# Performance work log

Measured on AMD Instinct MI355X. Metric: run time of the kernel, lower is better.

The kernel has to match this reference:

```python
import jax, jax.numpy as jnp
import numpy as np

DIM = 128
HEADS = 4


def setup_inputs() -> dict:
    key = jax.random.key(0)
    ks = jax.random.split(key, 6)
    B_, N, C = 2048, 49, DIM
    nW = 64
    x = jax.random.normal(ks[0], (B_, N, C), dtype=jnp.float32)
    mask = jax.random.normal(ks[1], (nW, N, N), dtype=jnp.float32)
    qkv_w = jax.random.normal(ks[2], (3 * C, C), dtype=jnp.float32) * 0.02
    qkv_b = jnp.zeros((3 * C,), dtype=jnp.float32)
    proj_w = jax.random.normal(ks[3], (C, C), dtype=jnp.float32) * 0.02
    proj_b = jnp.zeros((C,), dtype=jnp.float32)
    return {"x": x, "mask": mask, "qkv_w": qkv_w, "qkv_b": qkv_b,
            "proj_w": proj_w, "proj_b": proj_b}


def reference(x, mask, qkv_w, qkv_b, proj_w, proj_b):
    B_, N, C = x.shape
    H = HEADS
    Dh = C // H
    scale = Dh ** (-0.5)
    # fused QKV projection: [B_, N, 3C]
    qkv = x @ qkv_w.T + qkv_b
    qkv = qkv.reshape(B_, N, 3, H, Dh).transpose(2, 0, 3, 1, 4)  # [3, B_, H, N, Dh]
    q, k, v = qkv[0] * scale, qkv[1], qkv[2]
    attn = jnp.einsum('bhqd,bhkd->bhqk', q, k)  # [B_, H, N, N]
    nW = mask.shape[0]
    # add per-window additive mask: broadcast over images and heads
    attn = attn.reshape(B_ // nW, nW, H, N, N) + mask[None, :, None, :, :]
    attn = jax.nn.softmax(attn.reshape(B_, H, N, N), axis=-1)
    out = jnp.einsum('bhqk,bhkd->bhqd', attn, v)  # [B_, H, N, Dh]
    out = out.transpose(0, 2, 1, 3).reshape(B_, N, C)
    return out @ proj_w.T + proj_b
```

## Files before the change

kernel.cpp:

```cpp
#include <hip/hip_runtime.h>

typedef __bf16 bf16_t;
typedef __bf16 bf16x2 __attribute__((ext_vector_type(2)));
typedef __bf16 bf16x4 __attribute__((ext_vector_type(4)));
typedef __bf16 bf16x8 __attribute__((ext_vector_type(8)));
typedef float  f32x4  __attribute__((ext_vector_type(4)));

#define MFMA16(a, b, c) __builtin_amdgcn_mfma_f32_16x16x32_bf16((a), (b), (c), 0, 0, 0)

#define SMEM_BYTES 76800


__global__ void wconv_kernel(const float* __restrict__ qw, const float* __restrict__ pw,
                             bf16_t* __restrict__ o) {
    int i = (blockIdx.x * 256 + threadIdx.x) * 4;
    const float* src = (i < 49152) ? (qw + i) : (pw + (i - 49152));
    float4 f = *(const float4*)src;
    bf16x4 h;
    h[0] = (bf16_t)f.x; h[1] = (bf16_t)f.y; h[2] = (bf16_t)f.z; h[3] = (bf16_t)f.w;
    *(bf16x4*)(o + i) = h;
}

__device__ __forceinline__ bf16x8 ldw(const float* __restrict__ wf,
                                      const bf16_t* __restrict__ wb,
                                      int use_b, int idx) {
    if (use_b) {
        return *(const bf16x8*)(wb + idx);
    } else {
        float4 f0 = *(const float4*)(wf + idx);
        float4 f1 = *(const float4*)(wf + idx + 4);
        bf16x8 r;
        r[0] = (bf16_t)f0.x; r[1] = (bf16_t)f0.y; r[2] = (bf16_t)f0.z; r[3] = (bf16_t)f0.w;
        r[4] = (bf16_t)f1.x; r[5] = (bf16_t)f1.y; r[6] = (bf16_t)f1.z; r[7] = (bf16_t)f1.w;
        return r;
    }
}

__global__ __launch_bounds__(512, 4) void winattn_kernel(
    const float* __restrict__ xg, const float* __restrict__ maskg,
    const float* __restrict__ qwg, const float* __restrict__ qbg,
    const float* __restrict__ pwg, const float* __restrict__ pbg,
    const bf16_t* __restrict__ wqb, const bf16_t* __restrict__ wpb,
    const int use_wbf, const int nW, float* __restrict__ outg)
{
    extern __shared__ char smem[];
    bf16_t* xatt  = (bf16_t*)smem;
    float*  maskl = (float*)smem;

    const int b    = blockIdx.x;
    const int tid  = threadIdx.x;
    const int w    = tid >> 6;
    const int lane = tid & 63;
    const int g    = lane >> 4;
    const int c0   = lane & 15;

    {
        const float4* xb = (const float4*)(xg + (long)b * 6272);
        #pragma unroll 4
        for (int i = tid; i < 1568; i += 512) {
            float4 f = xb[i];
            int row = i >> 5;
            int col = (i & 31) << 2;
            bf16x4 h;
            h[0] = (bf16_t)f.x; h[1] = (bf16_t)f.y; h[2] = (bf16_t)f.z; h[3] = (bf16_t)f.w;
            *(bf16x4*)(xatt + row * 136 + col) = h;
        }
        unsigned int* z = (unsigned int*)(xatt + 49 * 136);
        for (int i = tid; i < 1020; i += 512) z[i] = 0u;
    }
    __syncthreads();

    {
        f32x4 acc[3][4];
        #pragma unroll
        for (int nt = 0; nt < 3; ++nt)
            #pragma unroll
            for (int mt = 0; mt < 4; ++mt) acc[nt][mt] = {0.f, 0.f, 0.f, 0.f};

        #pragma unroll
        for (int ks = 0; ks < 4; ++ks) {
            bf16x8 a[4];
            #pragma unroll
            for (int mt = 0; mt < 4; ++mt)
                a[mt] = *(const bf16x8*)(xatt + (mt * 16 + c0) * 136 + ks * 32 + g * 8);
            #pragma unroll
            for (int nt = 0; nt < 3; ++nt) {
                int o   = (w * 3 + nt) * 16 + c0;
                bf16x8 bb = ldw(qwg, wqb, use_wbf, o * 128 + ks * 32 + g * 8);
                #pragma unroll
                for (int mt = 0; mt < 4; ++mt)
                    acc[nt][mt] = MFMA16(a[mt], bb, acc[nt][mt]);
            }
        }
        #pragma unroll
        for (int nt = 0; nt < 3; ++nt) {
            int og   = (w * 3 + nt) * 16;
            float bias = qbg[og + c0];
            int part = og >> 7;
            int rem  = og & 127;
            int hh   = rem >> 5;
            int dh   = (rem & 31) + c0;
            bf16_t* hb = (bf16_t*)(smem + 17408 + hh * 14848);
            #pragma unroll
            for (int mt = 0; mt < 4; ++mt) {
                #pragma unroll
                for (int r = 0; r < 4; ++r) {
                    int row   = mt * 16 + g * 4 + r;
                    float val = acc[nt][mt][r] + bias;
                    if (part == 0)      hb[row * 40 + dh]        = (bf16_t)val;
                    else if (part == 1) hb[2560 + row * 40 + dh] = (bf16_t)val;
                    else                hb[5120 + dh * 72 + row] = (bf16_t)val;
                }
            }
        }
    }
    __syncthreads();

    {
        const float* mb = maskg + (long)(b % nW) * 2401;
        for (int i = tid; i < 2401; i += 512)
            maskl[(i / 49) * 52 + (i % 49)] = mb[i];
    }
    __syncthreads();

    const int h   = w >> 1;
    const int qh2 = w & 1;
    bf16_t* qls = (bf16_t*)(smem + 17408 + h * 14848);
    bf16_t* kls = qls + 2560;
    bf16_t* vls = qls + 5120;
    bf16_t* pls = qls;
    bf16x8 ka[4], qb2[2];
    #pragma unroll
    for (int mt = 0; mt < 4; ++mt)
        ka[mt] = *(const bf16x8*)(kls + (mt * 16 + c0) * 40 + g * 8);
    #pragma unroll
    for (int nt = 0; nt < 2; ++nt)
        qb2[nt] = *(const bf16x8*)(qls + ((qh2 * 2 + nt) * 16 + c0) * 40 + g * 8);
    __syncthreads();

    {
        f32x4 s[2][4];
        #pragma unroll
        for (int nt = 0; nt < 2; ++nt)
            #pragma unroll
            for (int mt = 0; mt < 4; ++mt) s[nt][mt] = {0.f, 0.f, 0.f, 0.f};
        #pragma unroll
        for (int nt = 0; nt < 2; ++nt)
            #pragma unroll
            for (int mt = 0; mt < 4; ++mt)
                s[nt][mt] = MFMA16(ka[mt], qb2[nt], s[nt][mt]);

        const float scale = 0.17677669529663687f;
        #pragma unroll
        for (int nt = 0; nt < 2; ++nt) {
            int q  = (qh2 * 2 + nt) * 16 + c0;
            int qm = q < 49 ? q : 48;
            float lg[16];
            float m = -1e30f;
            #pragma unroll
            for (int mt = 0; mt < 4; ++mt) {
                #pragma unroll
                for (int r = 0; r < 4; ++r) {
                    int kv  = mt * 16 + g * 4 + r;
                    float v = (kv < 49) ? (s[nt][mt][r] * scale + maskl[qm * 52 + kv])
                                        : -1e30f;
                    lg[mt * 4 + r] = v;
                    m = fmaxf(m, v);
                }
            }
            m = fmaxf(m, __shfl_xor(m, 16));
            m = fmaxf(m, __shfl_xor(m, 32));
            float sum = 0.f;
            #pragma unroll
            for (int i = 0; i < 16; ++i) { float e = __expf(lg[i] - m); lg[i] = e; sum += e; }
            sum += __shfl_xor(sum, 16);
            sum += __shfl_xor(sum, 32);
            float inv = 1.f / sum;
            #pragma unroll
            for (int mt = 0; mt < 4; ++mt) {
                #pragma unroll
                for (int j = 0; j < 2; ++j) {
                    bf16x2 t;
                    t[0] = (bf16_t)(lg[mt * 4 + 2 * j    ] * inv);
                    t[1] = (bf16_t)(lg[mt * 4 + 2 * j + 1] * inv);
                    *(bf16x2*)(pls + q * 72 + mt * 16 + g * 4 + 2 * j) = t;
                }
            }
        }
    }
    __syncthreads();

    {
        f32x4 oo[2][2];
        #pragma unroll
        for (int mt = 0; mt < 2; ++mt)
            #pragma unroll
            for (int nt = 0; nt < 2; ++nt) oo[mt][nt] = {0.f, 0.f, 0.f, 0.f};
        #pragma unroll
        for (int ks = 0; ks < 2; ++ks) {
            bf16x8 va[2], pb2[2];
            #pragma unroll
            for (int mt = 0; mt < 2; ++mt)
                va[mt] = *(const bf16x8*)(vls + (mt * 16 + c0) * 72 + ks * 32 + g * 8);
            #pragma unroll
            for (int nt = 0; nt < 2; ++nt)
                pb2[nt] = *(const bf16x8*)(pls + ((qh2 * 2 + nt) * 16 + c0) * 72 + ks * 32 + g * 8);
            #pragma unroll
            for (int mt = 0; mt < 2; ++mt)
                #pragma unroll
                for (int nt = 0; nt < 2; ++nt)
                    oo[mt][nt] = MFMA16(va[mt], pb2[nt], oo[mt][nt]);
        }
        #pragma unroll
        for (int nt = 0; nt < 2; ++nt) {
            int q = (qh2 * 2 + nt) * 16 + c0;
            #pragma unroll
            for (int mt = 0; mt < 2; ++mt) {
                #pragma unroll
                for (int j = 0; j < 2; ++j) {
                    bf16x2 t;
                    t[0] = (bf16_t)oo[mt][nt][2 * j];
                    t[1] = (bf16_t)oo[mt][nt][2 * j + 1];
                    *(bf16x2*)(xatt + q * 136 + h * 32 + mt * 16 + g * 4 + 2 * j) = t;
                }
            }
        }
    }
    __syncthreads();

    {
        f32x4 acc[4];
        #pragma unroll
        for (int mt = 0; mt < 4; ++mt) acc[mt] = {0.f, 0.f, 0.f, 0.f};
        int col = w * 16 + c0;
        #pragma unroll
        for (int ks = 0; ks < 4; ++ks) {
            bf16x8 a[4];
            #pragma unroll
            for (int mt = 0; mt < 4; ++mt)
                a[mt] = *(const bf16x8*)(xatt + (mt * 16 + c0) * 136 + ks * 32 + g * 8);
            bf16x8 bb = ldw(pwg, wpb, use_wbf, col * 128 + ks * 32 + g * 8);
            #pragma unroll
            for (int mt = 0; mt < 4; ++mt)
                acc[mt] = MFMA16(a[mt], bb, acc[mt]);
        }
        float pb = pbg[col];
        float* ob = outg + (long)b * 6272;
        #pragma unroll
        for (int mt = 0; mt < 4; ++mt) {
            #pragma unroll
            for (int r = 0; r < 4; ++r) {
                int q = mt * 16 + g * 4 + r;
                if (q < 49) ob[q * 128 + col] = acc[mt][r] + pb;
            }
        }
    }
}

extern "C" void kernel_launch(void* const* d_in, const int* in_sizes, int n_in,
                              void* d_out, int out_size, void* d_ws, size_t ws_size,
                              hipStream_t stream) {
    const float* xg  = (const float*)d_in[0];
    const float* mg  = (const float*)d_in[1];
    const float* qwg = (const float*)d_in[2];
    const float* qbg = (const float*)d_in[3];
    const float* pwg = (const float*)d_in[4];
    const float* pbg = (const float*)d_in[5];
    float* outg = (float*)d_out;

    const int B  = in_sizes[0] / (49 * 128);
    const int nW = in_sizes[1] / (49 * 49);

    int use_wbf = (d_ws != nullptr && ws_size >= 131072) ? 1 : 0;
    bf16_t* wqb = (bf16_t*)d_ws;
    bf16_t* wpb = use_wbf ? (wqb + 49152) : nullptr;
    if (use_wbf)
        wconv_kernel<<<64, 256, 0, stream>>>(qwg, pwg, wqb);

    (void)hipFuncSetAttribute((const void*)winattn_kernel,
                              hipFuncAttributeMaxDynamicSharedMemorySize, SMEM_BYTES);

    winattn_kernel<<<B, 512, SMEM_BYTES, stream>>>(
        xg, mg, qwg, qbg, pwg, pbg, wqb, use_wbf ? wpb : wqb, use_wbf, nW, outg);
}
```

Before: 75.12 us.

## Drop weight-convert kernel, swap MFMA operands, load mask into registers, vectorize stores

After: 87.71 us. 1.17x slower.

```diff
diff --git a/kernel.cpp b/kernel.cpp
--- a/kernel.cpp
+++ b/kernel.cpp
@@ -1,7 +1,6 @@
 #include <hip/hip_runtime.h>
 
 typedef __bf16 bf16_t;
-typedef __bf16 bf16x2 __attribute__((ext_vector_type(2)));
 typedef __bf16 bf16x4 __attribute__((ext_vector_type(4)));
 typedef __bf16 bf16x8 __attribute__((ext_vector_type(8)));
 typedef float  f32x4  __attribute__((ext_vector_type(4)));
@@ -11,41 +10,23 @@
 #define SMEM_BYTES 76800
 
 
-__global__ void wconv_kernel(const float* __restrict__ qw, const float* __restrict__ pw,
-                             bf16_t* __restrict__ o) {
-    int i = (blockIdx.x * 256 + threadIdx.x) * 4;
-    const float* src = (i < 49152) ? (qw + i) : (pw + (i - 49152));
-    float4 f = *(const float4*)src;
-    bf16x4 h;
-    h[0] = (bf16_t)f.x; h[1] = (bf16_t)f.y; h[2] = (bf16_t)f.z; h[3] = (bf16_t)f.w;
-    *(bf16x4*)(o + i) = h;
-}
-
-__device__ __forceinline__ bf16x8 ldw(const float* __restrict__ wf,
-                                      const bf16_t* __restrict__ wb,
-                                      int use_b, int idx) {
-    if (use_b) {
-        return *(const bf16x8*)(wb + idx);
-    } else {
-        float4 f0 = *(const float4*)(wf + idx);
-        float4 f1 = *(const float4*)(wf + idx + 4);
-        bf16x8 r;
-        r[0] = (bf16_t)f0.x; r[1] = (bf16_t)f0.y; r[2] = (bf16_t)f0.z; r[3] = (bf16_t)f0.w;
-        r[4] = (bf16_t)f1.x; r[5] = (bf16_t)f1.y; r[6] = (bf16_t)f1.z; r[7] = (bf16_t)f1.w;
-        return r;
-    }
+__device__ __forceinline__ bf16x8 ld8f(const float* __restrict__ p) {
+    float4 f0 = *(const float4*)p;
+    float4 f1 = *(const float4*)(p + 4);
+    bf16x8 r;
+    r[0] = (bf16_t)f0.x; r[1] = (bf16_t)f0.y; r[2] = (bf16_t)f0.z; r[3] = (bf16_t)f0.w;
+    r[4] = (bf16_t)f1.x; r[5] = (bf16_t)f1.y; r[6] = (bf16_t)f1.z; r[7] = (bf16_t)f1.w;
+    return r;
 }
 
 __global__ __launch_bounds__(512, 4) void winattn_kernel(
     const float* __restrict__ xg, const float* __restrict__ maskg,
     const float* __restrict__ qwg, const float* __restrict__ qbg,
     const float* __restrict__ pwg, const float* __restrict__ pbg,
-    const bf16_t* __restrict__ wqb, const bf16_t* __restrict__ wpb,
-    const int use_wbf, const int nW, float* __restrict__ outg)
+    const int nW, float* __restrict__ outg)
 {
     extern __shared__ char smem[];
-    bf16_t* xatt  = (bf16_t*)smem;
-    float*  maskl = (float*)smem;
+    bf16_t* xatt = (bf16_t*)smem;
 
     const int b    = blockIdx.x;
     const int tid  = threadIdx.x;
@@ -71,6 +52,12 @@
     __syncthreads();
 
     {
+        const int orow0 = 48 * w;
+        float4 bias[3];
+        #pragma unroll
+        for (int nt = 0; nt < 3; ++nt)
+            bias[nt] = *(const float4*)(qbg + orow0 + 16 * nt + 4 * g);
+
         f32x4 acc[3][4];
         #pragma unroll
         for (int nt = 0; nt < 3; ++nt)
@@ -79,47 +66,50 @@
 
         #pragma unroll
         for (int ks = 0; ks < 4; ++ks) {
-            bf16x8 a[4];
-            #pragma unroll
-            for (int mt = 0; mt < 4; ++mt)
-                a[mt] = *(const bf16x8*)(xatt + (mt * 16 + c0) * 136 + ks * 32 + g * 8);
-            #pragma unroll
-            for (int nt = 0; nt < 3; ++nt) {
-                int o   = (w * 3 + nt) * 16 + c0;
-                bf16x8 bb = ldw(qwg, wqb, use_wbf, o * 128 + ks * 32 + g * 8);
+            bf16x8 wfk[3];
+            #pragma unroll
+            for (int nt = 0; nt < 3; ++nt)
+                wfk[nt] = ld8f(qwg + (orow0 + 16 * nt + c0) * 128 + 32 * ks + 8 * g);
+            bf16x8 xf[4];
+            #pragma unroll
+            for (int mt = 0; mt < 4; ++mt)
+                xf[mt] = *(const bf16x8*)(xatt + (16 * mt + c0) * 136 + 32 * ks + 8 * g);
+            #pragma unroll
+            for (int nt = 0; nt < 3; ++nt)
                 #pragma unroll
                 for (int mt = 0; mt < 4; ++mt)
-                    acc[nt][mt] = MFMA16(a[mt], bb, acc[nt][mt]);
-            }
-        }
+                    acc[nt][mt] = MFMA16(wfk[nt], xf[mt], acc[nt][mt]);
+        }
+
         #pragma unroll
         for (int nt = 0; nt < 3; ++nt) {
-            int og   = (w * 3 + nt) * 16;
-            float bias = qbg[og + c0];
-            int part = og >> 7;
-            int rem  = og & 127;
+            int o0   = orow0 + 16 * nt + 4 * g;
+            int part = (orow0 + 16 * nt) >> 7;
+            int rem  = o0 & 127;
             int hh   = rem >> 5;
-            int dh   = (rem & 31) + c0;
+            int dh0  = rem & 31;
             bf16_t* hb = (bf16_t*)(smem + 17408 + hh * 14848);
             #pragma unroll
             for (int mt = 0; mt < 4; ++mt) {
-                #pragma unroll
-                for (int r = 0; r < 4; ++r) {
-                    int row   = mt * 16 + g * 4 + r;
-                    float val = acc[nt][mt][r] + bias;
-                    if (part == 0)      hb[row * 40 + dh]        = (bf16_t)val;
-                    else if (part == 1) hb[2560 + row * 40 + dh] = (bf16_t)val;
-                    else                hb[5120 + dh * 72 + row] = (bf16_t)val;
+                int tok = 16 * mt + c0;
+                bf16x4 t;
+                t[0] = (bf16_t)(acc[nt][mt][0] + bias[nt].x);
+                t[1] = (bf16_t)(acc[nt][mt][1] + bias[nt].y);
+                t[2] = (bf16_t)(acc[nt][mt][2] + bias[nt].z);
+                t[3] = (bf16_t)(acc[nt][mt][3] + bias[nt].w);
+                if (part == 0) {
+                    *(bf16x4*)(hb + tok * 40 + dh0) = t;
+                } else if (part == 1) {
+                    *(bf16x4*)(hb + 2560 + tok * 40 + dh0) = t;
+                } else {
+                    bf16_t* vt = hb + 5120;
+                    vt[(dh0 + 0) * 72 + tok] = t[0];
+                    vt[(dh0 + 1) * 72 + tok] = t[1];
+                    vt[(dh0 + 2) * 72 + tok] = t[2];
+                    vt[(dh0 + 3) * 72 + tok] = t[3];
                 }
             }
         }
-    }
-    __syncthreads();
-
-    {
-        const float* mb = maskg + (long)(b % nW) * 2401;
-        for (int i = tid; i < 2401; i += 512)
-            maskl[(i / 49) * 52 + (i % 49)] = mb[i];
     }
     __syncthreads();
 
@@ -129,45 +119,56 @@
     bf16_t* kls = qls + 2560;
     bf16_t* vls = qls + 5120;
     bf16_t* pls = qls;
+
+    float mvals[2][16];
+    {
+        const float* mrow = maskg + (long)(b % nW) * 2401;
+        #pragma unroll
+        for (int nt = 0; nt < 2; ++nt) {
+            int q  = (qh2 * 2 + nt) * 16 + c0;
+            int qm = q < 49 ? q : 48;
+            const float* mr = mrow + qm * 49;
+            #pragma unroll
+            for (int mt = 0; mt < 4; ++mt)
+                #pragma unroll
+                for (int r = 0; r < 4; ++r) {
+                    int kv = 16 * mt + 4 * g + r;
+                    mvals[nt][mt * 4 + r] = (kv < 49) ? mr[kv] : -1e30f;
+                }
+        }
+    }
+
     bf16x8 ka[4], qb2[2];
     #pragma unroll
     for (int mt = 0; mt < 4; ++mt)
-        ka[mt] = *(const bf16x8*)(kls + (mt * 16 + c0) * 40 + g * 8);
+        ka[mt] = *(const bf16x8*)(kls + (16 * mt + c0) * 40 + 8 * g);
     #pragma unroll
     for (int nt = 0; nt < 2; ++nt)
-        qb2[nt] = *(const bf16x8*)(qls + ((qh2 * 2 + nt) * 16 + c0) * 40 + g * 8);
-    __syncthreads();
-
-    {
-        f32x4 s[2][4];
-        #pragma unroll
-        for (int nt = 0; nt < 2; ++nt)
-            #pragma unroll
-            for (int mt = 0; mt < 4; ++mt) s[nt][mt] = {0.f, 0.f, 0.f, 0.f};
-        #pragma unroll
-        for (int nt = 0; nt < 2; ++nt)
-            #pragma unroll
-            for (int mt = 0; mt < 4; ++mt)
-                s[nt][mt] = MFMA16(ka[mt], qb2[nt], s[nt][mt]);
-
+        qb2[nt] = *(const bf16x8*)(qls + ((qh2 * 2 + nt) * 16 + c0) * 40 + 8 * g);
+    __syncthreads();
+
+    {
         const float scale = 0.17677669529663687f;
         #pragma unroll
         for (int nt = 0; nt < 2; ++nt) {
-            int q  = (qh2 * 2 + nt) * 16 + c0;
-            int qm = q < 49 ? q : 48;
+            f32x4 s[4];
+            #pragma unroll
+            for (int mt = 0; mt < 4; ++mt) s[mt] = {0.f, 0.f, 0.f, 0.f};
+            #pragma unroll
+            for (int mt = 0; mt < 4; ++mt)
+                s[mt] = MFMA16(ka[mt], qb2[nt], s[mt]);
+
+            int q = (qh2 * 2 + nt) * 16 + c0;
             float lg[16];
             float m = -1e30f;
             #pragma unroll
-            for (int mt = 0; mt < 4; ++mt) {
+            for (int mt = 0; mt < 4; ++mt)
                 #pragma unroll
                 for (int r = 0; r < 4; ++r) {
-                    int kv  = mt * 16 + g * 4 + r;
-                    float v = (kv < 49) ? (s[nt][mt][r] * scale + maskl[qm * 52 + kv])
-                                        : -1e30f;
+                    float v = s[mt][r] * scale + mvals[nt][mt * 4 + r];
                     lg[mt * 4 + r] = v;
                     m = fmaxf(m, v);
                 }
-            }
             m = fmaxf(m, __shfl_xor(m, 16));
             m = fmaxf(m, __shfl_xor(m, 32));
             float sum = 0.f;
@@ -178,19 +179,25 @@
             float inv = 1.f / sum;
             #pragma unroll
             for (int mt = 0; mt < 4; ++mt) {
-                #pragma unroll
-                for (int j = 0; j < 2; ++j) {
-                    bf16x2 t;
-                    t[0] = (bf16_t)(lg[mt * 4 + 2 * j    ] * inv);
-                    t[1] = (bf16_t)(lg[mt * 4 + 2 * j + 1] * inv);
-                    *(bf16x2*)(pls + q * 72 + mt * 16 + g * 4 + 2 * j) = t;
-                }
-            }
-        }
-    }
-    __syncthreads();
-
-    {
+                bf16x4 t;
+                t[0] = (bf16_t)(lg[mt * 4 + 0] * inv);
+                t[1] = (bf16_t)(lg[mt * 4 + 1] * inv);
+                t[2] = (bf16_t)(lg[mt * 4 + 2] * inv);
+                t[3] = (bf16_t)(lg[mt * 4 + 3] * inv);
+                *(bf16x4*)(pls + q * 72 + 16 * mt + 4 * g) = t;
+            }
+        }
+    }
+    __syncthreads();
+
+    bf16x8 pwf[4];
+    float4 pbias;
+    {
+        #pragma unroll
+        for (int ks = 0; ks < 4; ++ks)
+            pwf[ks] = ld8f(pwg + (16 * w + c0) * 128 + 32 * ks + 8 * g);
+        pbias = *(const float4*)(pbg + 16 * w + 4 * g);
+
         f32x4 oo[2][2];
         #pragma unroll
         for (int mt = 0; mt < 2; ++mt)
@@ -198,31 +205,30 @@
             for (int nt = 0; nt < 2; ++nt) oo[mt][nt] = {0.f, 0.f, 0.f, 0.f};
         #pragma unroll
         for (int ks = 0; ks < 2; ++ks) {
-            bf16x8 va[2], pb2[2];
+            bf16x8 va[2], pf[2];
             #pragma unroll
             for (int mt = 0; mt < 2; ++mt)
-                va[mt] = *(const bf16x8*)(vls + (mt * 16 + c0) * 72 + ks * 32 + g * 8);
+                va[mt] = *(const bf16x8*)(vls + (16 * mt + c0) * 72 + 32 * ks + 8 * g);
             #pragma unroll
             for (int nt = 0; nt < 2; ++nt)
-                pb2[nt] = *(const bf16x8*)(pls + ((qh2 * 2 + nt) * 16 + c0) * 72 + ks * 32 + g * 8);
+                pf[nt] = *(const bf16x8*)(pls + ((qh2 * 2 + nt) * 16 + c0) * 72 + 32 * ks + 8 * g);
             #pragma unroll
             for (int mt = 0; mt < 2; ++mt)
                 #pragma unroll
                 for (int nt = 0; nt < 2; ++nt)
-                    oo[mt][nt] = MFMA16(va[mt], pb2[nt], oo[mt][nt]);
+                    oo[mt][nt] = MFMA16(va[mt], pf[nt], oo[mt][nt]);
         }
         #pragma unroll
         for (int nt = 0; nt < 2; ++nt) {
             int q = (qh2 * 2 + nt) * 16 + c0;
             #pragma unroll
             for (int mt = 0; mt < 2; ++mt) {
-                #pragma unroll
-                for (int j = 0; j < 2; ++j) {
-                    bf16x2 t;
-                    t[0] = (bf16_t)oo[mt][nt][2 * j];
-                    t[1] = (bf16_t)oo[mt][nt][2 * j + 1];
-                    *(bf16x2*)(xatt + q * 136 + h * 32 + mt * 16 + g * 4 + 2 * j) = t;
-                }
+                bf16x4 t;
+                t[0] = (bf16_t)oo[mt][nt][0];
+                t[1] = (bf16_t)oo[mt][nt][1];
+                t[2] = (bf16_t)oo[mt][nt][2];
+                t[3] = (bf16_t)oo[mt][nt][3];
+                *(bf16x4*)(xatt + q * 136 + h * 32 + 16 * mt + 4 * g) = t;
             }
         }
     }
@@ -232,26 +238,27 @@
         f32x4 acc[4];
         #pragma unroll
         for (int mt = 0; mt < 4; ++mt) acc[mt] = {0.f, 0.f, 0.f, 0.f};
-        int col = w * 16 + c0;
         #pragma unroll
         for (int ks = 0; ks < 4; ++ks) {
-            bf16x8 a[4];
-            #pragma unroll
-            for (int mt = 0; mt < 4; ++mt)
-                a[mt] = *(const bf16x8*)(xatt + (mt * 16 + c0) * 136 + ks * 32 + g * 8);
-            bf16x8 bb = ldw(pwg, wpb, use_wbf, col * 128 + ks * 32 + g * 8);
-            #pragma unroll
-            for (int mt = 0; mt < 4; ++mt)
-                acc[mt] = MFMA16(a[mt], bb, acc[mt]);
-        }
-        float pb = pbg[col];
+            bf16x8 af[4];
+            #pragma unroll
+            for (int mt = 0; mt < 4; ++mt)
+                af[mt] = *(const bf16x8*)(xatt + (16 * mt + c0) * 136 + 32 * ks + 8 * g);
+            #pragma unroll
+            for (int mt = 0; mt < 4; ++mt)
+                acc[mt] = MFMA16(pwf[ks], af[mt], acc[mt]);
+        }
         float* ob = outg + (long)b * 6272;
         #pragma unroll
         for (int mt = 0; mt < 4; ++mt) {
-            #pragma unroll
-            for (int r = 0; r < 4; ++r) {
-                int q = mt * 16 + g * 4 + r;
-                if (q < 49) ob[q * 128 + col] = acc[mt][r] + pb;
+            int tok = 16 * mt + c0;
+            if (tok < 49) {
+                float4 t;
+                t.x = acc[mt][0] + pbias.x;
+                t.y = acc[mt][1] + pbias.y;
+                t.z = acc[mt][2] + pbias.z;
+                t.w = acc[mt][3] + pbias.w;
+                *(float4*)(ob + tok * 128 + 16 * w + 4 * g) = t;
             }
         }
     }
@@ -271,15 +278,9 @@
     const int B  = in_sizes[0] / (49 * 128);
     const int nW = in_sizes[1] / (49 * 49);
 
-    int use_wbf = (d_ws != nullptr && ws_size >= 131072) ? 1 : 0;
-    bf16_t* wqb = (bf16_t*)d_ws;
-    bf16_t* wpb = use_wbf ? (wqb + 49152) : nullptr;
-    if (use_wbf)
-        wconv_kernel<<<64, 256, 0, stream>>>(qwg, pwg, wqb);
-
     (void)hipFuncSetAttribute((const void*)winattn_kernel,
                               hipFuncAttributeMaxDynamicSharedMemorySize, SMEM_BYTES);
 
     winattn_kernel<<<B, 512, SMEM_BYTES, stream>>>(
-        xg, mg, qwg, qbg, pwg, pbg, wqb, use_wbf ? wpb : wqb, use_wbf, nW, outg);
+        xg, mg, qwg, qbg, pwg, pbg, nW, outg);
 }
```

## Keep softmax probabilities in registers and read mask directly from global memory

Applied to the files above, without the earlier changes.

Result: faster. 64.55 us (-14.1%).

```diff
diff --git a/kernel.cpp b/kernel.cpp
--- a/kernel.cpp
+++ b/kernel.cpp
@@ -5,11 +5,21 @@
 typedef __bf16 bf16x4 __attribute__((ext_vector_type(4)));
 typedef __bf16 bf16x8 __attribute__((ext_vector_type(8)));
 typedef float  f32x4  __attribute__((ext_vector_type(4)));
+typedef float  f32x4u __attribute__((ext_vector_type(4), aligned(4)));
+typedef unsigned int u32;
 
 #define MFMA16(a, b, c) __builtin_amdgcn_mfma_f32_16x16x32_bf16((a), (b), (c), 0, 0, 0)
 
 #define SMEM_BYTES 76800
 
+
+union W8 { u32 u[4]; bf16x8 v; };
+
+__device__ __forceinline__ u32 pack2(float a, float b) {
+    union { bf16x2 h; u32 u; } c;
+    c.h[0] = (bf16_t)a; c.h[1] = (bf16_t)b;
+    return c.u;
+}
 
 __global__ void wconv_kernel(const float* __restrict__ qw, const float* __restrict__ pw,
                              bf16_t* __restrict__ o) {
@@ -44,8 +54,7 @@
     const int use_wbf, const int nW, float* __restrict__ outg)
 {
     extern __shared__ char smem[];
-    bf16_t* xatt  = (bf16_t*)smem;
-    float*  maskl = (float*)smem;
+    bf16_t* xatt = (bf16_t*)smem;
 
     const int b    = blockIdx.x;
     const int tid  = threadIdx.x;
@@ -61,9 +70,9 @@
             float4 f = xb[i];
             int row = i >> 5;
             int col = (i & 31) << 2;
-            bf16x4 h;
-            h[0] = (bf16_t)f.x; h[1] = (bf16_t)f.y; h[2] = (bf16_t)f.z; h[3] = (bf16_t)f.w;
-            *(bf16x4*)(xatt + row * 136 + col) = h;
+            bf16x4 hq;
+            hq[0] = (bf16_t)f.x; hq[1] = (bf16_t)f.y; hq[2] = (bf16_t)f.z; hq[3] = (bf16_t)f.w;
+            *(bf16x4*)(xatt + row * 136 + col) = hq;
         }
         unsigned int* z = (unsigned int*)(xatt + 49 * 136);
         for (int i = tid; i < 1020; i += 512) z[i] = 0u;
@@ -71,55 +80,74 @@
     __syncthreads();
 
     {
-        f32x4 acc[3][4];
-        #pragma unroll
-        for (int nt = 0; nt < 3; ++nt)
-            #pragma unroll
-            for (int mt = 0; mt < 4; ++mt) acc[nt][mt] = {0.f, 0.f, 0.f, 0.f};
+        const int oqk = 32 * w;
+        float4 biasqk[2];
+        #pragma unroll
+        for (int nt = 0; nt < 2; ++nt)
+            biasqk[nt] = *(const float4*)(qbg + oqk + 16 * nt + 4 * g);
+        float biasv = qbg[256 + 16 * w + c0];
+        const float scale = 0.17677669529663687f;
+        const float qmul  = (w < 4) ? scale : 1.0f;
+
+        f32x4 aqk[2][4], av[4];
+        #pragma unroll
+        for (int nt = 0; nt < 2; ++nt)
+            #pragma unroll
+            for (int mt = 0; mt < 4; ++mt) aqk[nt][mt] = {0.f, 0.f, 0.f, 0.f};
+        #pragma unroll
+        for (int mt = 0; mt < 4; ++mt) av[mt] = {0.f, 0.f, 0.f, 0.f};
 
         #pragma unroll
         for (int ks = 0; ks < 4; ++ks) {
-            bf16x8 a[4];
+            bf16x8 wqk[2], wv;
+            #pragma unroll
+            for (int nt = 0; nt < 2; ++nt)
+                wqk[nt] = ldw(qwg, wqb, use_wbf, (oqk + 16 * nt + c0) * 128 + 32 * ks + 8 * g);
+            wv = ldw(qwg, wqb, use_wbf, (256 + 16 * w + c0) * 128 + 32 * ks + 8 * g);
+            bf16x8 xf[4];
             #pragma unroll
             for (int mt = 0; mt < 4; ++mt)
-                a[mt] = *(const bf16x8*)(xatt + (mt * 16 + c0) * 136 + ks * 32 + g * 8);
-            #pragma unroll
-            for (int nt = 0; nt < 3; ++nt) {
-                int o   = (w * 3 + nt) * 16 + c0;
-                bf16x8 bb = ldw(qwg, wqb, use_wbf, o * 128 + ks * 32 + g * 8);
+                xf[mt] = *(const bf16x8*)(xatt + (16 * mt + c0) * 136 + 32 * ks + 8 * g);
+            #pragma unroll
+            for (int nt = 0; nt < 2; ++nt)
                 #pragma unroll
                 for (int mt = 0; mt < 4; ++mt)
-                    acc[nt][mt] = MFMA16(a[mt], bb, acc[nt][mt]);
-            }
-        }
-        #pragma unroll
-        for (int nt = 0; nt < 3; ++nt) {
-            int og   = (w * 3 + nt) * 16;
-            float bias = qbg[og + c0];
-            int part = og >> 7;
-            int rem  = og & 127;
-            int hh   = rem >> 5;
-            int dh   = (rem & 31) + c0;
-            bf16_t* hb = (bf16_t*)(smem + 17408 + hh * 14848);
+                    aqk[nt][mt] = MFMA16(wqk[nt], xf[mt], aqk[nt][mt]);
+            #pragma unroll
+            for (int mt = 0; mt < 4; ++mt)
+                av[mt] = MFMA16(xf[mt], wv, av[mt]);
+        }
+
+        #pragma unroll
+        for (int nt = 0; nt < 2; ++nt) {
+            int oh  = (oqk + 16 * nt) & 127;
+            int hh  = oh >> 5;
+            int dh0 = 16 * nt  + 4 * g;
+            bf16_t* base = (bf16_t*)(smem + 17408 + hh * 14848) + (w < 4 ? 0 : 2560);
             #pragma unroll
             for (int mt = 0; mt < 4; ++mt) {
-                #pragma unroll
-                for (int r = 0; r < 4; ++r) {
-                    int row   = mt * 16 + g * 4 + r;
-                    float val = acc[nt][mt][r] + bias;
-                    if (part == 0)      hb[row * 40 + dh]        = (bf16_t)val;
-                    else if (part == 1) hb[2560 + row * 40 + dh] = (bf16_t)val;
-                    else                hb[5120 + dh * 72 + row] = (bf16_t)val;
-                }
-            }
-        }
-    }
-    __syncthreads();
-
-    {
-        const float* mb = maskg + (long)(b % nW) * 2401;
-        for (int i = tid; i < 2401; i += 512)
-            maskl[(i / 49) * 52 + (i % 49)] = mb[i];
+                int tok = 16 * mt + c0;
+                bf16x4 t;
+                t[0] = (bf16_t)((aqk[nt][mt][0] + biasqk[nt].x) * qmul);
+                t[1] = (bf16_t)((aqk[nt][mt][1] + biasqk[nt].y) * qmul);
+                t[2] = (bf16_t)((aqk[nt][mt][2] + biasqk[nt].z) * qmul);
+                t[3] = (bf16_t)((aqk[nt][mt][3] + biasqk[nt].w) * qmul);
+                *(bf16x4*)(base + tok * 40 + dh0) = t;
+            }
+        }
+        {
+            int dhv = 16 * (w & 1) + c0;
+            bf16_t* vt = (bf16_t*)(smem + 17408 + (w >> 1) * 14848) + 5120;
+            #pragma unroll
+            for (int mt = 0; mt < 4; ++mt) {
+                bf16x4 t;
+                t[0] = (bf16_t)(av[mt][0] + biasv);
+                t[1] = (bf16_t)(av[mt][1] + biasv);
+                t[2] = (bf16_t)(av[mt][2] + biasv);
+                t[3] = (bf16_t)(av[mt][3] + biasv);
+                *(bf16x4*)(vt + dhv * 72 + 16 * mt + 4 * g) = t;
+            }
+        }
     }
     __syncthreads();
 
@@ -128,130 +156,158 @@
     bf16_t* qls = (bf16_t*)(smem + 17408 + h * 14848);
     bf16_t* kls = qls + 2560;
     bf16_t* vls = qls + 5120;
-    bf16_t* pls = qls;
+
+    bf16x8 pwf[4];
+    #pragma unroll
+    for (int ks = 0; ks < 4; ++ks)
+        pwf[ks] = ldw(pwg, wpb, use_wbf, (16 * w + c0) * 128 + 32 * ks + 8 * g);
+    float4 pbias4 = *(const float4*)(pbg + 16 * w + 4 * g);
+
+    float mv[2][16];
+    {
+        const float* mrow = maskg + (long)(b % nW) * 2401;
+        #pragma unroll
+        for (int nt = 0; nt < 2; ++nt) {
+            int q  = (qh2 * 2 + nt) * 16 + c0;
+            int qm = q < 49 ? q : 48;
+            const float* mr = mrow + qm * 49;
+            f32x4u m0 = *(const f32x4u*)(mr + 4 * g);
+            f32x4u m1 = *(const f32x4u*)(mr + 16 + 4 * g);
+            f32x4u m2 = *(const f32x4u*)(mr + 32 + 4 * g);
+            float m48 = mr[48];
+            #pragma unroll
+            for (int r = 0; r < 4; ++r) {
+                mv[nt][0 + r] = m0[r];
+                mv[nt][4 + r] = m1[r];
+                mv[nt][8 + r] = m2[r];
+            }
+            mv[nt][12] = (g == 0) ? m48 : -1e30f;
+            mv[nt][13] = -1e30f; mv[nt][14] = -1e30f; mv[nt][15] = -1e30f;
+        }
+    }
+
     bf16x8 ka[4], qb2[2];
     #pragma unroll
     for (int mt = 0; mt < 4; ++mt)
-        ka[mt] = *(const bf16x8*)(kls + (mt * 16 + c0) * 40 + g * 8);
+        ka[mt] = *(const bf16x8*)(kls + (16 * mt + c0) * 40 + 8 * g);
     #pragma unroll
     for (int nt = 0; nt < 2; ++nt)
-        qb2[nt] = *(const bf16x8*)(qls + ((qh2 * 2 + nt) * 16 + c0) * 40 + g * 8);
-    __syncthreads();
-
-    {
-        f32x4 s[2][4];
+        qb2[nt] = *(const bf16x8*)(qls + ((qh2 * 2 + nt) * 16 + c0) * 40 + 8 * g);
+
+    bf16x8 pa[2][2];
+    const bool gl = (g & 1) != 0, gh = (g & 2) != 0;
+    #pragma unroll
+    for (int nt = 0; nt < 2; ++nt) {
+        f32x4 s[4];
+        #pragma unroll
+        for (int mt = 0; mt < 4; ++mt) s[mt] = {0.f, 0.f, 0.f, 0.f};
+        #pragma unroll
+        for (int mt = 0; mt < 4; ++mt)
+            s[mt] = MFMA16(ka[mt], qb2[nt], s[mt]);
+
+        float lg[16];
+        float m = -1e30f;
+        #pragma unroll
+        for (int mt = 0; mt < 4; ++mt)
+            #pragma unroll
+            for (int r = 0; r < 4; ++r) {
+                float v = s[mt][r] + mv[nt][mt * 4 + r];
+                lg[mt * 4 + r] = v;
+                m = fmaxf(m, v);
+            }
+        m = fmaxf(m, __shfl_xor(m, 16));
+        m = fmaxf(m, __shfl_xor(m, 32));
+        float sum = 0.f;
+        #pragma unroll
+        for (int i = 0; i < 16; ++i) { float e = __expf(lg[i] - m); lg[i] = e; sum += e; }
+        sum += __shfl_xor(sum, 16);
+        sum += __shfl_xor(sum, 32);
+        float inv = 1.f / sum;
+
+        u32 wd[8];
+        #pragma unroll
+        for (int j = 0; j < 8; ++j) {
+            int mt = j >> 1, rb = (j & 1) * 2;
+            wd[j] = pack2(lg[mt * 4 + rb] * inv, lg[mt * 4 + rb + 1] * inv);
+        }
+        u32 X[8], Y[8], Z[8];
+        #pragma unroll
+        for (int j = 0; j < 8; ++j) X[j] = __shfl_xor(wd[j], 16);
+        #pragma unroll
+        for (int j = 0; j < 8; ++j) Y[j] = __shfl_xor(wd[j], 32);
+        #pragma unroll
+        for (int j = 0; j < 8; ++j) Z[j] = __shfl_xor(X[j], 32);
+        #pragma unroll
+        for (int ks = 0; ks < 2; ++ks) {
+            W8 u;
+            #pragma unroll
+            for (int t = 0; t < 4; ++t) {
+                int j0 = 4 * ks + (t & 1);
+                int j1 = j0 + 2;
+                u32 lo, hi;
+                if (t < 2) { lo = gl ? Z[j0] : wd[j0]; hi = gl ? X[j1] : Y[j1]; }
+                else       { lo = gl ? Y[j0] : X[j0];  hi = gl ? wd[j1] : Z[j1]; }
+                u.u[t] = gh ? hi : lo;
+            }
+            pa[nt][ks] = u.v;
+        }
+    }
+
+    {
+        f32x4 o2[2][2];
         #pragma unroll
         for (int nt = 0; nt < 2; ++nt)
             #pragma unroll
-            for (int mt = 0; mt < 4; ++mt) s[nt][mt] = {0.f, 0.f, 0.f, 0.f};
+            for (int dt = 0; dt < 2; ++dt) o2[nt][dt] = {0.f, 0.f, 0.f, 0.f};
+        #pragma unroll
+        for (int ks = 0; ks < 2; ++ks) {
+            bf16x8 vf[2];
+            #pragma unroll
+            for (int dt = 0; dt < 2; ++dt)
+                vf[dt] = *(const bf16x8*)(vls + (16 * dt + c0) * 72 + 32 * ks + 8 * g);
+            #pragma unroll
+            for (int nt = 0; nt < 2; ++nt)
+                #pragma unroll
+                for (int dt = 0; dt < 2; ++dt)
+                    o2[nt][dt] = MFMA16(pa[nt][ks], vf[dt], o2[nt][dt]);
+        }
         #pragma unroll
         for (int nt = 0; nt < 2; ++nt)
             #pragma unroll
-            for (int mt = 0; mt < 4; ++mt)
-                s[nt][mt] = MFMA16(ka[mt], qb2[nt], s[nt][mt]);
-
-        const float scale = 0.17677669529663687f;
-        #pragma unroll
-        for (int nt = 0; nt < 2; ++nt) {
-            int q  = (qh2 * 2 + nt) * 16 + c0;
-            int qm = q < 49 ? q : 48;
-            float lg[16];
-            float m = -1e30f;
-            #pragma unroll
-            for (int mt = 0; mt < 4; ++mt) {
+            for (int dt = 0; dt < 2; ++dt)
                 #pragma unroll
                 for (int r = 0; r < 4; ++r) {
-                    int kv  = mt * 16 + g * 4 + r;
-                    float v = (kv < 49) ? (s[nt][mt][r] * scale + maskl[qm * 52 + kv])
-                                        : -1e30f;
-                    lg[mt * 4 + r] = v;
-                    m = fmaxf(m, v);
+                    int q = (qh2 * 2 + nt) * 16 + 4 * g + r;
+                    xatt[q * 136 + 32 * h + 16 * dt + c0] = (bf16_t)o2[nt][dt][r];
                 }
-            }
-            m = fmaxf(m, __shfl_xor(m, 16));
-            m = fmaxf(m, __shfl_xor(m, 32));
-            float sum = 0.f;
-            #pragma unroll
-            for (int i = 0; i < 16; ++i) { float e = __expf(lg[i] - m); lg[i] = e; sum += e; }
-            sum += __shfl_xor(sum, 16);
-            sum += __shfl_xor(sum, 32);
-            float inv = 1.f / sum;
-            #pragma unroll
-            for (int mt = 0; mt < 4; ++mt) {
-                #pragma unroll
-                for (int j = 0; j < 2; ++j) {
-                    bf16x2 t;
-                    t[0] = (bf16_t)(lg[mt * 4 + 2 * j    ] * inv);
-                    t[1] = (bf16_t)(lg[mt * 4 + 2 * j + 1] * inv);
-                    *(bf16x2*)(pls + q * 72 + mt * 16 + g * 4 + 2 * j) = t;
-                }
-            }
-        }
     }
     __syncthreads();
 
     {
-        f32x4 oo[2][2];
-        #pragma unroll
-        for (int mt = 0; mt < 2; ++mt)
-            #pragma unroll
-            for (int nt = 0; nt < 2; ++nt) oo[mt][nt] = {0.f, 0.f, 0.f, 0.f};
-        #pragma unroll
-        for (int ks = 0; ks < 2; ++ks) {
-            bf16x8 va[2], pb2[2];
-            #pragma unroll
-            for (int mt = 0; mt < 2; ++mt)
-                va[mt] = *(const bf16x8*)(vls + (mt * 16 + c0) * 72 + ks * 32 + g * 8);
-            #pragma unroll
-            for (int nt = 0; nt < 2; ++nt)
-                pb2[nt] = *(const bf16x8*)(pls + ((qh2 * 2 + nt) * 16 + c0) * 72 + ks * 32 + g * 8);
-            #pragma unroll
-            for (int mt = 0; mt < 2; ++mt)
-                #pragma unroll
-                for (int nt = 0; nt < 2; ++nt)
-                    oo[mt][nt] = MFMA16(va[mt], pb2[nt], oo[mt][nt]);
-        }
-        #pragma unroll
-        for (int nt = 0; nt < 2; ++nt) {
-            int q = (qh2 * 2 + nt) * 16 + c0;
-            #pragma unroll
-            for (int mt = 0; mt < 2; ++mt) {
-                #pragma unroll
-                for (int j = 0; j < 2; ++j) {
-                    bf16x2 t;
-                    t[0] = (bf16_t)oo[mt][nt][2 * j];
-                    t[1] = (bf16_t)oo[mt][nt][2 * j + 1];
-                    *(bf16x2*)(xatt + q * 136 + h * 32 + mt * 16 + g * 4 + 2 * j) = t;
-                }
-            }
-        }
-    }
-    __syncthreads();
-
-    {
         f32x4 acc[4];
         #pragma unroll
         for (int mt = 0; mt < 4; ++mt) acc[mt] = {0.f, 0.f, 0.f, 0.f};
-        int col = w * 16 + c0;
         #pragma unroll
         for (int ks = 0; ks < 4; ++ks) {
-            bf16x8 a[4];
+            bf16x8 af[4];
             #pragma unroll
             for (int mt = 0; mt < 4; ++mt)
-                a[mt] = *(const bf16x8*)(xatt + (mt * 16 + c0) * 136 + ks * 32 + g * 8);
-            bf16x8 bb = ldw(pwg, wpb, use_wbf, col * 128 + ks * 32 + g * 8);
+                af[mt] = *(const bf16x8*)(xatt + (16 * mt + c0) * 136 + 32 * ks + 8 * g);
             #pragma unroll
             for (int mt = 0; mt < 4; ++mt)
-                acc[mt] = MFMA16(a[mt], bb, acc[mt]);
-        }
-        float pb = pbg[col];
+                acc[mt] = MFMA16(pwf[ks], af[mt], acc[mt]);
+        }
         float* ob = outg + (long)b * 6272;
         #pragma unroll
         for (int mt = 0; mt < 4; ++mt) {
-            #pragma unroll
-            for (int r = 0; r < 4; ++r) {
-                int q = mt * 16 + g * 4 + r;
-                if (q < 49) ob[q * 128 + col] = acc[mt][r] + pb;
+            int tok = 16 * mt + c0;
+            if (tok < 49) {
+                float4 t;
+                t.x = acc[mt][0] + pbias4.x;
+                t.y = acc[mt][1] + pbias4.y;
+                t.z = acc[mt][2] + pbias4.z;
+                t.w = acc[mt][3] + pbias4.w;
+                *(float4*)(ob + tok * 128 + 16 * w + 4 * g) = t;
             }
         }
     }
```
